# Performance work log

Hardware: AMD Instinct MI355X
Metric: run time of the kernel (lower is better)

Reference implementation:

```python
import jax, jax.numpy as jnp
import numpy as np

B, T, DIM = 2, 2048, 1024
H, DH, E, K = 16, 64, 8, 2


def setup_inputs() -> dict:
    key = jax.random.key(0)
    ks = jax.random.split(key, 7)
    s = 0.02
    return {
        "x":  jax.random.normal(ks[0], (B, T, DIM), jnp.float32),
        "Wq": jax.random.normal(ks[1], (H, DH, DIM), jnp.float32) * s,  # Linear(dim -> h*dh), reshaped
        "Wk": jax.random.normal(ks[2], (H, DH, DIM), jnp.float32) * s,
        "Wv": jax.random.normal(ks[3], (E, DH, DIM), jnp.float32) * s,  # per-expert Linear(dim -> dh)
        "Ws": jax.random.normal(ks[4], (H, E, DIM), jnp.float32) * s,   # V-gate Linear(dim -> h*e)
        "Wd": jax.random.normal(ks[5], (H, E, DIM), jnp.float32) * s,   # O-gate Linear(dim -> h*e)
        "Wo": jax.random.normal(ks[6], (E, DIM, DH), jnp.float32) * s,  # per-expert Linear(dh -> dim)
    }


def reference(x, Wq, Wk, Wv, Ws, Wd, Wo):
    scale = DH ** -0.5
    # projections: [b,h,t,dh]
    q = jnp.einsum('btc,hdc->bhtd', x, Wq)
    k = jnp.einsum('btc,hdc->bhtd', x, Wk)

    # ---- compute_moe (V experts): top-k gate, sigmoid weights ----
    gate_v = jnp.einsum('btc,hec->bthe', x, Ws)              # [b,t,h,e]
    w, sel = jax.lax.top_k(gate_v, K)                        # [b,t,h,K]
    wsig = jax.nn.sigmoid(w)
    oh = jax.nn.one_hot(sel, E, dtype=x.dtype)               # [b,t,h,K,e]
    mix_v = jnp.einsum('bthk,bthke->bthe', wsig, oh)         # weighted routing mask
    proj_v = jnp.einsum('btc,edc->bted', x, Wv)              # all-expert V projections (E small)
    v = jnp.einsum('bthe,bted->bhtd', mix_v, proj_v)         # [b,h,t,dh]

    # ---- standard attention core ----
    scores = jnp.einsum('bhid,bhjd->bhij', q * scale, k)     # [b,h,t,t]
    probs = jax.nn.softmax(scores, axis=-1)
    attn = jnp.einsum('bhij,bhjd->bihd', probs, v)           # [b,t,h,dh]

    # ---- compute_moe_o (O experts): top-k gate; NOTE original never uses its
    # softmax weights, so selected experts are summed UNWEIGHTED ----
    gate_o = jnp.einsum('btc,hec->bthe', x, Wd)
    _, sel_o = jax.lax.top_k(gate_o, K)
    mask_o = jax.nn.one_hot(sel_o, E, dtype=x.dtype).sum(axis=3)  # [b,t,h,e] in {0,1}
    res = jnp.einsum('bthe,bthd,efd->bthf', mask_o, attn, Wo)     # [b,t,h,dim]
    return res.sum(axis=2)                                        # [b,t,dim]
```

## Files before the change

kernel.cpp:

```cpp
#include <hip/hip_runtime.h>
#include <math.h>

#define TSEQ 2048
#define NB   2
#define NH   16
#define NE   8
#define DHD  64
#define MDIM 1024
#define MBT  4096
#define LDQKV 2560
#define GTAU 1e-3f
#define MAXFLAG 16384

typedef __attribute__((ext_vector_type(8))) short bf16x8;
typedef __attribute__((ext_vector_type(4))) float f32x4;
typedef __attribute__((ext_vector_type(16))) float f32x16;
typedef unsigned int u32;

__device__ inline unsigned short f2bf(float f) {
    union { float f; unsigned u; } v; v.f = f;
    unsigned r = v.u + 0x7fff + ((v.u >> 16) & 1);
    return (unsigned short)(r >> 16);
}
__device__ inline float bf2f(unsigned short h) {
    union { unsigned u; float f; } v; v.u = ((unsigned)h) << 16;
    return v.f;
}
__device__ inline u32 cvtpk(float a, float b) {
    u32 r;
    asm("v_cvt_pk_bf16_f32 %0, %1, %2" : "=v"(r) : "v"(a), "v"(b));
    return r;
}
__device__ inline float fexp2(float x) {
#if __has_builtin(__builtin_amdgcn_exp2f)
    return __builtin_amdgcn_exp2f(x);
#else
    float r; asm("v_exp_f32 %0, %1" : "=v"(r) : "v"(x)); return r;
#endif
}

__device__ inline void gload16(const void* g, void* l) {
    __builtin_amdgcn_global_load_lds((const __attribute__((address_space(1))) u32*)g,
                                     (__attribute__((address_space(3))) u32*)l, 16, 0, 0);
}

__device__ inline void cast8s(const float* __restrict__ in, unsigned short* __restrict__ out,
                              int i, float sc) {
    const float4* p = (const float4*)(in + (size_t)i * 8);
    float4 a = p[0], b = p[1];
    unsigned short o[8] = { f2bf(a.x*sc), f2bf(a.y*sc), f2bf(a.z*sc), f2bf(a.w*sc),
                            f2bf(b.x*sc), f2bf(b.y*sc), f2bf(b.z*sc), f2bf(b.w*sc) };
    *(uint4*)(out + (size_t)i * 8) = *(const uint4*)o;
}
__device__ inline void cast8hl(const float* __restrict__ in,
                               unsigned short* __restrict__ oh, unsigned short* __restrict__ ol,
                               int i) {
    const float4* p = (const float4*)(in + (size_t)i * 8);
    float4 a = p[0], b = p[1];
    float f[8] = { a.x, a.y, a.z, a.w, b.x, b.y, b.z, b.w };
    unsigned short h8[8], l8[8];
    #pragma unroll
    for (int j = 0; j < 8; ++j) {
        unsigned short hi = f2bf(f[j]);
        h8[j] = hi;
        l8[j] = f2bf(f[j] - bf2f(hi));
    }
    *(uint4*)(oh + (size_t)i * 8) = *(const uint4*)h8;
    *(uint4*)(ol + (size_t)i * 8) = *(const uint4*)l8;
}

__global__ __launch_bounds__(256)
void prep(const float* __restrict__ x,  const float* __restrict__ Wq,
          const float* __restrict__ Wk, const float* __restrict__ Wv,
          const float* __restrict__ Ws, const float* __restrict__ Wd,
          const float* __restrict__ Wo,
          unsigned short* __restrict__ xb, unsigned short* __restrict__ xbl,
          unsigned short* __restrict__ Wqkvb,
          unsigned short* __restrict__ Wsdh, unsigned short* __restrict__ Wsdl,
          unsigned short* __restrict__ WoTh, unsigned short* __restrict__ WoTl,
          u32* __restrict__ flags)
{
    const float qsc = 0.125f * 1.4426950408889634f;
    int b = blockIdx.x, tid = threadIdx.x;
    if (b == 0 && tid == 0) flags[0] = 0;
    if (b < 2048)      cast8hl(x, xb, xbl,          (b        ) * 256 + tid);
    else if (b < 2560) cast8s(Wq, Wqkvb,            (b - 2048) * 256 + tid, qsc);
    else if (b < 3072) cast8s(Wk, Wqkvb + 1048576,  (b - 2560) * 256 + tid, 1.f);
    else if (b < 3328) cast8s(Wv, Wqkvb + 2097152,  (b - 3072) * 256 + tid, 1.f);
    else if (b < 3456) {
        int i = (b - 3328) * 256 + tid;
        const float* src = (i < 16384) ? Ws + (size_t)i * 8 : Wd + (size_t)(i - 16384) * 8;
        const float4* p = (const float4*)src;
        float4 a = p[0], bq = p[1];
        float f8[8] = { a.x, a.y, a.z, a.w, bq.x, bq.y, bq.z, bq.w };
        unsigned short h8[8], l8[8];
        #pragma unroll
        for (int j = 0; j < 8; ++j) {
            unsigned short hi = f2bf(f8[j]);
            h8[j] = hi;
            l8[j] = f2bf(f8[j] - bf2f(hi));
        }
        *(uint4*)(Wsdh + (size_t)i * 8) = *(const uint4*)h8;
        *(uint4*)(Wsdl + (size_t)i * 8) = *(const uint4*)l8;
    } else {
        int idx = (b - 3456) * 256 + tid;
        int f = idx >> 9, ed = idx & 511, e = ed >> 6, d = ed & 63;
        float v = Wo[(size_t)e * (MDIM * DHD) + (size_t)f * DHD + d];
        unsigned short hi = f2bf(v);
        WoTh[idx] = hi;
        WoTl[idx] = f2bf(v - bf2f(hi));
    }
}

__global__ __launch_bounds__(256)
void mfma_gemm(const unsigned short* __restrict__ A,
               const unsigned short* __restrict__ B,
               unsigned short* __restrict__ C, int N, int K, int nbx)
{
    __shared__ __align__(16) unsigned short As[128 * 32];
    __shared__ __align__(16) unsigned short Bs[128 * 32];
    const int o = blockIdx.x;
    const int q8 = (int)gridDim.x >> 3;
    const int virt = (o & 7) * q8 + (o >> 3);
    const int bx = virt % nbx, by = virt / nbx;
    const int tid = threadIdx.x;
    const int lane = tid & 63, wave = tid >> 6;
    const int m0 = by * 128, n0 = bx * 128;
    const int wm = (wave >> 1) * 64, wn = (wave & 1) * 64;
    const int fr = lane & 15, fg = lane >> 4;
    const int grow = lane >> 2, gcol = (lane & 3) * 8;

    f32x4 acc[4][4];
    #pragma unroll
    for (int i = 0; i < 4; ++i)
        #pragma unroll
        for (int j = 0; j < 4; ++j) acc[i][j] = (f32x4)0.f;

    for (int k0 = 0; k0 < K; k0 += 32) {
        __syncthreads();
        const unsigned short* gA = A + (size_t)(m0 + wave * 32 + grow) * K + k0 + gcol;
        gload16(gA,                 As + wave * 1024);
        gload16(gA + (size_t)16 * K, As + wave * 1024 + 512);
        const unsigned short* gB = B + (size_t)(n0 + wave * 32 + grow) * K + k0 + gcol;
        gload16(gB,                 Bs + wave * 1024);
        gload16(gB + (size_t)16 * K, Bs + wave * 1024 + 512);
        __syncthreads();
        bf16x8 af[4], bfr[4];
        #pragma unroll
        for (int t = 0; t < 4; ++t) {
            af[t]  = *(const bf16x8*)(As + (wm + t * 16 + fr) * 32 + fg * 8);
            bfr[t] = *(const bf16x8*)(Bs + (wn + t * 16 + fr) * 32 + fg * 8);
        }
        #pragma unroll
        for (int i = 0; i < 4; ++i)
            #pragma unroll
            for (int j = 0; j < 4; ++j)
                acc[i][j] = __builtin_amdgcn_mfma_f32_16x16x32_bf16(af[i], bfr[j], acc[i][j], 0, 0, 0);
    }
    #pragma unroll
    for (int i = 0; i < 4; ++i)
        #pragma unroll
        for (int j = 0; j < 4; ++j)
            #pragma unroll
            for (int rr = 0; rr < 4; ++rr) {
                int row = m0 + wm + i * 16 + fg * 4 + rr;
                int col = n0 + wn + j * 16 + fr;
                C[(size_t)row * N + col] = f2bf(acc[i][j][rr]);
            }
}

__global__ __launch_bounds__(256)
void mfma_gemm3(const unsigned short* __restrict__ Ah, const unsigned short* __restrict__ Al,
                const unsigned short* __restrict__ Bh, const unsigned short* __restrict__ Bl,
                float* __restrict__ C)
{
    const int Kc = 512, N = 1024;
    __shared__ __align__(16) unsigned short Ash[128 * 32];
    __shared__ __align__(16) unsigned short Asl[128 * 32];
    __shared__ __align__(16) unsigned short Bsh[128 * 32];
    __shared__ __align__(16) unsigned short Bsl[128 * 32];
    const int o = blockIdx.x;
    const int virt = (o & 7) * 32 + (o >> 3);
    const int bx = virt & 7, by = virt >> 3;
    const int tid = threadIdx.x;
    const int lane = tid & 63, wave = tid >> 6;
    const int m0 = by * 128, n0 = bx * 128;
    const int wm = (wave >> 1) * 64, wn = (wave & 1) * 64;
    const int fr = lane & 15, fg = lane >> 4;
    const int grow = lane >> 2, gcol = (lane & 3) * 8;

    f32x4 acc[4][4];
    #pragma unroll
    for (int i = 0; i < 4; ++i)
        #pragma unroll
        for (int j = 0; j < 4; ++j) acc[i][j] = (f32x4)0.f;

    for (int k0 = 0; k0 < Kc; k0 += 32) {
        __syncthreads();
        const size_t roff  = (size_t)(m0 + wave * 32 + grow) * Kc + k0 + gcol;
        const size_t roffB = (size_t)(n0 + wave * 32 + grow) * Kc + k0 + gcol;
        gload16(Ah + roff,             Ash + wave * 1024);
        gload16(Ah + roff + 16 * Kc,   Ash + wave * 1024 + 512);
        gload16(Al + roff,             Asl + wave * 1024);
        gload16(Al + roff + 16 * Kc,   Asl + wave * 1024 + 512);
        gload16(Bh + roffB,            Bsh + wave * 1024);
        gload16(Bh + roffB + 16 * Kc,  Bsh + wave * 1024 + 512);
        gload16(Bl + roffB,            Bsl + wave * 1024);
        gload16(Bl + roffB + 16 * Kc,  Bsl + wave * 1024 + 512);
        __syncthreads();
        bf16x8 ah[4], al[4], bh[4], bl[4];
        #pragma unroll
        for (int t = 0; t < 4; ++t) {
            ah[t] = *(const bf16x8*)(Ash + (wm + t * 16 + fr) * 32 + fg * 8);
            al[t] = *(const bf16x8*)(Asl + (wm + t * 16 + fr) * 32 + fg * 8);
            bh[t] = *(const bf16x8*)(Bsh + (wn + t * 16 + fr) * 32 + fg * 8);
            bl[t] = *(const bf16x8*)(Bsl + (wn + t * 16 + fr) * 32 + fg * 8);
        }
        #pragma unroll
        for (int i = 0; i < 4; ++i)
            #pragma unroll
            for (int j = 0; j < 4; ++j) {
                acc[i][j] = __builtin_amdgcn_mfma_f32_16x16x32_bf16(ah[i], bh[j], acc[i][j], 0, 0, 0);
                acc[i][j] = __builtin_amdgcn_mfma_f32_16x16x32_bf16(ah[i], bl[j], acc[i][j], 0, 0, 0);
                acc[i][j] = __builtin_amdgcn_mfma_f32_16x16x32_bf16(al[i], bh[j], acc[i][j], 0, 0, 0);
            }
    }
    #pragma unroll
    for (int i = 0; i < 4; ++i)
        #pragma unroll
        for (int j = 0; j < 4; ++j)
            #pragma unroll
            for (int rr = 0; rr < 4; ++rr) {
                int row = m0 + wm + i * 16 + fg * 4 + rr;
                int col = n0 + wn + j * 16 + fr;
                C[(size_t)row * N + col] = acc[i][j][rr];
            }
}

__global__ __launch_bounds__(256)
void gate_gemm(const unsigned short* __restrict__ Ah, const unsigned short* __restrict__ Al,
               const unsigned short* __restrict__ Bh, const unsigned short* __restrict__ Bl,
               float* __restrict__ C)
{
    const int K = 1024, N = 256;
    __shared__ __align__(16) unsigned short S[4][64 * 32];
    const int tid = threadIdx.x;
    const int lane = tid & 63, wave = tid >> 6;
    const int m0 = blockIdx.y * 64, n0 = blockIdx.x * 64;
    const int wm = (wave >> 1) * 32, wn = (wave & 1) * 32;
    const int fr = lane & 15, fg = lane >> 4;
    const int grow = lane >> 2, gcol = (lane & 3) * 8;

    const unsigned short* src = (wave == 0) ? Ah : (wave == 1) ? Al : (wave == 2) ? Bh : Bl;
    const int brow = (wave >= 2) ? n0 : m0;

    f32x4 acc[2][2];
    #pragma unroll
    for (int i = 0; i < 2; ++i)
        #pragma unroll
        for (int j = 0; j < 2; ++j) acc[i][j] = (f32x4)0.f;

    for (int k0 = 0; k0 < K; k0 += 32) {
        __syncthreads();
        #pragma unroll
        for (int i = 0; i < 4; ++i)
            gload16(src + (size_t)(brow + i * 16 + grow) * K + k0 + gcol, &S[wave][i * 512]);
        __syncthreads();
        bf16x8 ah[2], al[2], bh[2], bl[2];
        #pragma unroll
        for (int t = 0; t < 2; ++t) {
            ah[t] = *(const bf16x8*)(&S[0][(wm + t * 16 + fr) * 32 + fg * 8]);
            al[t] = *(const bf16x8*)(&S[1][(wm + t * 16 + fr) * 32 + fg * 8]);
            bh[t] = *(const bf16x8*)(&S[2][(wn + t * 16 + fr) * 32 + fg * 8]);
            bl[t] = *(const bf16x8*)(&S[3][(wn + t * 16 + fr) * 32 + fg * 8]);
        }
        #pragma unroll
        for (int i = 0; i < 2; ++i)
            #pragma unroll
            for (int j = 0; j < 2; ++j) {
                acc[i][j] = __builtin_amdgcn_mfma_f32_16x16x32_bf16(ah[i], bh[j], acc[i][j], 0, 0, 0);
                acc[i][j] = __builtin_amdgcn_mfma_f32_16x16x32_bf16(ah[i], bl[j], acc[i][j], 0, 0, 0);
                acc[i][j] = __builtin_amdgcn_mfma_f32_16x16x32_bf16(al[i], bh[j], acc[i][j], 0, 0, 0);
            }
    }
    #pragma unroll
    for (int i = 0; i < 2; ++i)
        #pragma unroll
        for (int j = 0; j < 2; ++j)
            #pragma unroll
            for (int rr = 0; rr < 4; ++rr) {
                int row = m0 + wm + i * 16 + fg * 4 + rr;
                int col = n0 + wn + j * 16 + fr;
                C[(size_t)row * N + col] = acc[i][j][rr];
            }
}

__global__ __launch_bounds__(256)
void gate_topk2(const float* __restrict__ Gf,
                float2* __restrict__ wv, u32* __restrict__ selv, u32* __restrict__ selo,
                u32* __restrict__ flags)
{
    int item = blockIdx.x * 256 + threadIdx.x;
    int bt = item >> 4, h = item & 15;
    const float* g = Gf + (size_t)bt * 256 + h * NE;
    float b1 = -1e30f, b2 = -1e30f, b3 = -1e30f; int e1 = 0, e2 = 0;
    #pragma unroll
    for (int e = 0; e < NE; ++e) {
        float v = g[e];
        if (v > b1)      { b3 = b2; b2 = b1; e2 = e1; b1 = v; e1 = e; }
        else if (v > b2) { b3 = b2; b2 = v;  e2 = e; }
        else if (v > b3) { b3 = v; }
    }
    wv[item] = make_float2(1.f / (1.f + __expf(-b1)), 1.f / (1.f + __expf(-b2)));
    selv[item] = (u32)e1 | ((u32)e2 << 4);
    if (b2 - b3 < GTAU) {
        u32 p = atomicAdd(flags, 1u);
        if (p < MAXFLAG) flags[1 + p] = (u32)item;
    }
    const float* go = g + 128;
    float o1 = -1e30f, o2 = -1e30f, o3 = -1e30f; int f1 = 0, f2 = 0;
    #pragma unroll
    for (int e = 0; e < NE; ++e) {
        float v = go[e];
        if (v > o1)      { o3 = o2; o2 = o1; f2 = f1; o1 = v; f1 = e; }
        else if (v > o2) { o3 = o2; o2 = v;  f2 = e; }
        else if (v > o3) { o3 = v; }
    }
    selo[item] = (1u << f1) | (1u << f2);
    if (o2 - o3 < GTAU) {
        u32 p = atomicAdd(flags, 1u);
        if (p < MAXFLAG) flags[1 + p] = (u32)item | 0x10000u;
    }
}

__global__ __launch_bounds__(256)
void gate_fix(const float* __restrict__ x, const float* __restrict__ Ws,
              const float* __restrict__ Wd, const u32* __restrict__ flags,
              float2* __restrict__ wv, u32* __restrict__ selv, u32* __restrict__ selo)
{
    u32 nf = flags[0]; if (nf > MAXFLAG) nf = MAXFLAG;
    int gw = (blockIdx.x * 256 + threadIdx.x) >> 6;
    int lane = threadIdx.x & 63;
    int nwaves = gridDim.x * 4;
    for (u32 w = gw; w < nf; w += nwaves) {
        u32 rec = flags[1 + w];
        int item = rec & 0xffff, which = rec >> 16;
        int bt = item >> 4, h = item & 15;
        const float* W = (which ? Wd : Ws) + (size_t)h * NE * MDIM + lane * 16;
        const float* xr = x + (size_t)bt * MDIM + lane * 16;
        double g[8];
        #pragma unroll
        for (int e = 0; e < 8; ++e) {
            double s = 0.0;
            #pragma unroll
            for (int c = 0; c < 16; ++c)
                s += (double)xr[c] * (double)W[(size_t)e * MDIM + c];
            g[e] = s;
        }
        #pragma unroll
        for (int off = 32; off; off >>= 1)
            #pragma unroll
            for (int e = 0; e < 8; ++e)
                g[e] += __shfl_xor(g[e], off, 64);
        if (lane == 0) {
            double b1 = -1e300, b2 = -1e300; int i1 = 0, i2 = 0;
            #pragma unroll
            for (int e = 0; e < 8; ++e) {
                double v = g[e];
                if (v > b1)      { b2 = b1; i2 = i1; b1 = v; i1 = e; }
                else if (v > b2) { b2 = v;  i2 = e; }
            }
            if (which == 0) {
                wv[item] = make_float2(1.f / (1.f + __expf(-(float)b1)),
                                       1.f / (1.f + __expf(-(float)b2)));
                selv[item] = (u32)i1 | ((u32)i2 << 4);
            } else {
                selo[item] = (1u << i1) | (1u << i2);
            }
        }
    }
}

#define VTP 72
__global__ __launch_bounds__(256)
void vtrans(const unsigned short* __restrict__ QKVb, const float2* __restrict__ wv,
            const u32* __restrict__ selv, unsigned short* __restrict__ Vtg)
{
    __shared__ __align__(16) unsigned short Ls[256 * VTP];
    const int vid = blockIdx.x;
    const int xcd = vid & 7, local = vid >> 3;
    const int virt = xcd * 32 + local;
    const int b = virt >> 7, rem = virt & 127;
    const int tblk = rem >> 4, h = rem & 15;
    const int tid = threadIdx.x;

    {
        const int bt = b * TSEQ + tblk * 256 + tid;
        u32 s = selv[bt * 16 + h];
        float2 w = wv[bt * 16 + h];
        int e1 = s & 15, e2 = (s >> 4) & 15;
        const unsigned short* pv = QKVb + (size_t)bt * LDQKV + 2048;
        #pragma unroll
        for (int c = 0; c < 8; ++c) {
            uint4 a  = *(const uint4*)(pv + e1 * 64 + c * 8);
            uint4 bb = *(const uint4*)(pv + e2 * 64 + c * 8);
            unsigned short ea[8], eb[8], eo[8];
            *(uint4*)ea = a; *(uint4*)eb = bb;
            #pragma unroll
            for (int j = 0; j < 8; ++j)
                eo[j] = f2bf(w.x * bf2f(ea[j]) + w.y * bf2f(eb[j]));
            *(uint4*)(Ls + tid * VTP + c * 8) = *(const uint4*)eo;
        }
    }
    __syncthreads();
    {
        const int d = tid & 63, outer = tid >> 6;
        const size_t vrow = ((size_t)((b * NH + h) * DHD + d)) * TSEQ + tblk * 256;
        #pragma unroll
        for (int c8 = 0; c8 < 8; ++c8) {
            int t0 = (outer * 8 + c8) * 8;
            unsigned short o[8];
            #pragma unroll
            for (int j = 0; j < 8; ++j)
                o[j] = Ls[(t0 + j) * VTP + d];
            *(uint4*)(Vtg + vrow + t0) = *(const uint4*)o;
        }
    }
}

#define SPA 72
#define MFMA32(A,B,C) __builtin_amdgcn_mfma_f32_32x32x16_bf16(A, B, C, 0, 0, 0)
__global__ __launch_bounds__(256)
void attn_mfma(const unsigned short* __restrict__ QKVb,
               const unsigned short* __restrict__ Vtg,
               float* __restrict__ Op0, float* __restrict__ Op1,
               float* __restrict__ lp)
{
    __shared__ __align__(16) unsigned short Ks[64 * SPA];
    __shared__ __align__(16) unsigned short Vt[64 * SPA];
    const int vid = blockIdx.x;
    const int xcd = vid & 7, sl = vid >> 3;
    const int grp = xcd * 8 + (sl >> 4);
    const int q0  = (sl & 15) * 128;
    const int h   = grp & 15;
    const int z   = grp >> 4;
    const int b = z >> 1, split = z & 1;
    const int tid = threadIdx.x;
    const int lane = tid & 63, wq = tid >> 6;
    const int ql = lane & 31;
    const int hi = lane >> 5;
    const size_t base_q = ((size_t)b * TSEQ) * LDQKV + h * DHD;
    const size_t base_k = base_q + 1024;
    const size_t base_v = ((size_t)(b * NH + h) * DHD) * TSEQ;
    const int k00 = split * 1024;

    const int qrow = q0 + wq * 32 + ql;
    bf16x8 qa[4];
    #pragma unroll
    for (int t = 0; t < 4; ++t)
        qa[t] = *(const bf16x8*)(QKVb + base_q + (size_t)qrow * LDQKV + t * 16 + hi * 8);

    f32x16 o0 = (f32x16)0.f, o1 = (f32x16)0.f;
    float l_lane = 0.f;

    const int srow = tid >> 2, scol = (tid & 3) * 8;
    uint4 kr0 = *(const uint4*)(QKVb + base_k + (size_t)(k00 + srow) * LDQKV + scol);
    uint4 kr1 = *(const uint4*)(QKVb + base_k + (size_t)(k00 + srow) * LDQKV + scol + 32);
    uint4 vr0 = *(const uint4*)(Vtg + base_v + (size_t)srow * TSEQ + k00 + scol);
    uint4 vr1 = *(const uint4*)(Vtg + base_v + (size_t)srow * TSEQ + k00 + scol + 32);

    const int NT = 1024 / 64;
    for (int kb = 0; kb < NT; ++kb) {
        __syncthreads();
        *(uint4*)(Ks + srow * SPA + scol)      = kr0;
        *(uint4*)(Ks + srow * SPA + scol + 32) = kr1;
        *(uint4*)(Vt + srow * SPA + scol)      = vr0;
        *(uint4*)(Vt + srow * SPA + scol + 32) = vr1;
        __syncthreads();
        if (kb + 1 < NT) {
            const size_t gk = base_k + (size_t)(k00 + (kb + 1) * 64 + srow) * LDQKV + scol;
            const size_t gv = base_v + (size_t)srow * TSEQ + k00 + (kb + 1) * 64 + scol;
            kr0 = *(const uint4*)(QKVb + gk);
            kr1 = *(const uint4*)(QKVb + gk + 32);
            vr0 = *(const uint4*)(Vtg + gv);
            vr1 = *(const uint4*)(Vtg + gv + 32);
        }
        f32x16 s0 = (f32x16)0.f, s1 = (f32x16)0.f;
        #pragma unroll
        for (int t = 0; t < 4; ++t) {
            bf16x8 k0 = *(const bf16x8*)(Ks + ql * SPA + t * 16 + hi * 8);
            bf16x8 k1 = *(const bf16x8*)(Ks + (32 + ql) * SPA + t * 16 + hi * 8);
            s0 = MFMA32(k0, qa[t], s0);
            s1 = MFMA32(k1, qa[t], s1);
        }
        float ls0 = 0.f, ls1 = 0.f;
        u32 w[8];
        #pragma unroll
        for (int r = 0; r < 16; r += 2) {
            float pa = fexp2(s0[r]), pb = fexp2(s0[r + 1]);
            s0[r] = pa; s0[r + 1] = pb;
            ls0 += pa; ls1 += pb;
        }
        #pragma unroll
        for (int m = 0; m < 8; ++m) w[m] = cvtpk(s0[2*m], s0[2*m+1]);
        #pragma unroll
        for (int tl = 0; tl < 2; ++tl) {
            const int mb = 4 * tl, tk = tl;
            u32 send0 = hi ? w[mb]   : w[mb+2];
            u32 send1 = hi ? w[mb+1] : w[mb+3];
            u32 r0 = (u32)__shfl_xor((int)send0, 32, 64);
            u32 r1 = (u32)__shfl_xor((int)send1, 32, 64);
            union { u32 uw[4]; bf16x8 v; } pu;
            pu.uw[0] = hi ? r0 : w[mb];
            pu.uw[1] = hi ? r1 : w[mb+1];
            pu.uw[2] = hi ? w[mb+2] : r0;
            pu.uw[3] = hi ? w[mb+3] : r1;
            bf16x8 v0 = *(const bf16x8*)(Vt + ql * SPA + tk * 16 + hi * 8);
            bf16x8 v1 = *(const bf16x8*)(Vt + (32 + ql) * SPA + tk * 16 + hi * 8);
            o0 = MFMA32(pu.v, v0, o0);
            o1 = MFMA32(pu.v, v1, o1);
        }
        #pragma unroll
        for (int r = 0; r < 16; r += 2) {
            float pa = fexp2(s1[r]), pb = fexp2(s1[r + 1]);
            s1[r] = pa; s1[r + 1] = pb;
            ls0 += pa; ls1 += pb;
        }
        #pragma unroll
        for (int m = 0; m < 8; ++m) w[m] = cvtpk(s1[2*m], s1[2*m+1]);
        #pragma unroll
        for (int tl = 0; tl < 2; ++tl) {
            const int mb = 4 * tl, tk = 2 + tl;
            u32 send0 = hi ? w[mb]   : w[mb+2];
            u32 send1 = hi ? w[mb+1] : w[mb+3];
            u32 r0 = (u32)__shfl_xor((int)send0, 32, 64);
            u32 r1 = (u32)__shfl_xor((int)send1, 32, 64);
            union { u32 uw[4]; bf16x8 v; } pu;
            pu.uw[0] = hi ? r0 : w[mb];
            pu.uw[1] = hi ? r1 : w[mb+1];
            pu.uw[2] = hi ? w[mb+2] : r0;
            pu.uw[3] = hi ? w[mb+3] : r1;
            bf16x8 v0 = *(const bf16x8*)(Vt + ql * SPA + tk * 16 + hi * 8);
            bf16x8 v1 = *(const bf16x8*)(Vt + (32 + ql) * SPA + tk * 16 + hi * 8);
            o0 = MFMA32(pu.v, v0, o0);
            o1 = MFMA32(pu.v, v1, o1);
        }
        l_lane += ls0 + ls1;
    }
    float l_tot = l_lane + __shfl_xor(l_lane, 32, 64);
    float* Op = split ? Op1 : Op0;
    const size_t ob = ((size_t)b * TSEQ) * MDIM + h * DHD;
    #pragma unroll
    for (int r = 0; r < 16; ++r) {
        int qr = q0 + wq * 32 + (r & 3) + 8 * (r >> 2) + 4 * hi;
        Op[ob + (size_t)qr * MDIM + ql]      = o0[r];
        Op[ob + (size_t)qr * MDIM + 32 + ql] = o1[r];
    }
    if (hi == 0)
        lp[(((size_t)split * NB + b) * NH + h) * TSEQ + q0 + wq * 32 + ql] = l_tot;
}

__global__ __launch_bounds__(256)
void compute_U2(const float* __restrict__ Op0, const float* __restrict__ Op1,
                const float* __restrict__ lp, const u32* __restrict__ selo,
                unsigned short* __restrict__ Uh, unsigned short* __restrict__ Ul)
{
    int t = blockIdx.x * 256 + threadIdx.x;
    int bt = t >> 6, d = t & 63;
    int b = bt >> 11, ts = bt & 2047;
    float att[16];
    #pragma unroll
    for (int h = 0; h < NH; ++h) {
        size_t li = ((size_t)b * NH + h) * TSEQ + ts;
        float l = lp[li] + lp[li + (size_t)NB * NH * TSEQ];
        size_t oi = (size_t)bt * MDIM + h * DHD + d;
        att[h] = (Op0[oi] + Op1[oi]) / l;
    }
    const u32* sp = selo + bt * 16;
    u32 m[16];
    #pragma unroll
    for (int h = 0; h < NH; ++h) m[h] = sp[h];
    #pragma unroll
    for (int e = 0; e < NE; ++e) {
        float sum = 0.f;
        #pragma unroll
        for (int h = 0; h < NH; ++h)
            if (m[h] & (1u << e)) sum += att[h];
        int idx = bt * 512 + e * 64 + d;
        unsigned short hi16 = f2bf(sum);
        Uh[idx] = hi16;
        Ul[idx] = f2bf(sum - bf2f(hi16));
    }
}

extern "C" void kernel_launch(void* const* d_in, const int* in_sizes, int n_in,
                              void* d_out, int out_size, void* d_ws, size_t ws_size,
                              hipStream_t stream)
{
    const float* x  = (const float*)d_in[0];
    const float* Wq = (const float*)d_in[1];
    const float* Wk = (const float*)d_in[2];
    const float* Wv = (const float*)d_in[3];
    const float* Ws = (const float*)d_in[4];
    const float* Wd = (const float*)d_in[5];
    const float* Wo = (const float*)d_in[6];
    float* out = (float*)d_out;
    char* ws = (char*)d_ws;

    unsigned short* xb    = (unsigned short*)(ws);
    unsigned short* Wqkvb = (unsigned short*)(ws + 8388608);
    float*          Op0   = (float*)(ws);
    unsigned short* QKVb  = (unsigned short*)(ws + 16777216);
    unsigned short* Vtg   = (unsigned short*)(ws + 37748736);
    unsigned short* xbl   = (unsigned short*)(ws + 46137344);
    float*          Op1   = (float*)(ws + 46137344);
    float*          lp    = (float*)(ws + 62914560);
    unsigned short* WoTh  = (unsigned short*)(ws + 63438848);
    unsigned short* WoTl  = (unsigned short*)(ws + 64487424);
    float*          Gf    = (float*)(ws + 65536000);
    unsigned short* Uh    = (unsigned short*)(ws + 65536000);
    u32*            flags = (u32*)(ws + 69730304);
    unsigned short* Ul    = (unsigned short*)(ws + 69730304);
    float2*         wvp   = (float2*)(ws + 73924608);
    u32*            selv  = (u32*)(ws + 74448896);
    u32*            selo  = (u32*)(ws + 74711040);
    unsigned short* Wsdh  = (unsigned short*)(ws + 74973184);
    unsigned short* Wsdl  = (unsigned short*)(ws + 75497472);

    dim3 blk(256);
    prep<<<5504, blk, 0, stream>>>(x, Wq, Wk, Wv, Ws, Wd, Wo,
                                   xb, xbl, Wqkvb, Wsdh, Wsdl, WoTh, WoTl, flags);

    mfma_gemm<<<640, blk, 0, stream>>>(xb, Wqkvb, QKVb, LDQKV, 1024, 20);

    gate_gemm<<<dim3(4, 64), blk, 0, stream>>>(xb, xbl, Wsdh, Wsdl, Gf);
    gate_topk2<<<256, blk, 0, stream>>>(Gf, wvp, selv, selo, flags);
    gate_fix<<<64, blk, 0, stream>>>(x, Ws, Wd, flags, wvp, selv, selo);

    vtrans<<<256, blk, 0, stream>>>(QKVb, wvp, selv, Vtg);

    attn_mfma<<<1024, blk, 0, stream>>>(QKVb, Vtg, Op0, Op1, lp);

    compute_U2<<<1024, blk, 0, stream>>>(Op0, Op1, lp, selo, Uh, Ul);
    mfma_gemm3<<<256, blk, 0, stream>>>(Uh, Ul, WoTh, WoTl, out);
}
```

Baseline: 178.6 us.

## Fold gate projection into QKV GEMM with single-bf16 and wider fp32 fixup

The separate three-pass split-bf16 gate GEMM is removed. The Ws/Wd gate weights are appended as extra columns of the QKV weight matrix, so one GEMM launch produces Q, K, V and the gate logits, with the gate columns stored as fp32. Because gate logits are now computed in plain bf16, the top-k tie tolerance is widened and the fp32 fixup kernel gets more blocks and a larger flag capacity to recheck ambiguous routings. This saves a launch and the hi/lo conversions of x, but more tokens may need the exact fp32 recompute.

```diff
diff --git a/kernel.cpp b/kernel.cpp
--- a/kernel.cpp
+++ b/kernel.cpp
@@ -9,8 +9,9 @@
 #define MDIM 1024
 #define MBT  4096
 #define LDQKV 2560
-#define GTAU 1e-3f
-#define MAXFLAG 16384
+#define NFULL 2816
+#define GTAU 1.2e-2f
+#define MAXFLAG 32768
 
 typedef __attribute__((ext_vector_type(8))) short bf16x8;
 typedef __attribute__((ext_vector_type(4))) float f32x4;
@@ -52,38 +53,20 @@
                             f2bf(b.x*sc), f2bf(b.y*sc), f2bf(b.z*sc), f2bf(b.w*sc) };
     *(uint4*)(out + (size_t)i * 8) = *(const uint4*)o;
 }
-__device__ inline void cast8hl(const float* __restrict__ in,
-                               unsigned short* __restrict__ oh, unsigned short* __restrict__ ol,
-                               int i) {
-    const float4* p = (const float4*)(in + (size_t)i * 8);
-    float4 a = p[0], b = p[1];
-    float f[8] = { a.x, a.y, a.z, a.w, b.x, b.y, b.z, b.w };
-    unsigned short h8[8], l8[8];
-    #pragma unroll
-    for (int j = 0; j < 8; ++j) {
-        unsigned short hi = f2bf(f[j]);
-        h8[j] = hi;
-        l8[j] = f2bf(f[j] - bf2f(hi));
-    }
-    *(uint4*)(oh + (size_t)i * 8) = *(const uint4*)h8;
-    *(uint4*)(ol + (size_t)i * 8) = *(const uint4*)l8;
-}
 
 __global__ __launch_bounds__(256)
 void prep(const float* __restrict__ x,  const float* __restrict__ Wq,
           const float* __restrict__ Wk, const float* __restrict__ Wv,
           const float* __restrict__ Ws, const float* __restrict__ Wd,
           const float* __restrict__ Wo,
-          unsigned short* __restrict__ xb, unsigned short* __restrict__ xbl,
-          unsigned short* __restrict__ Wqkvb,
-          unsigned short* __restrict__ Wsdh, unsigned short* __restrict__ Wsdl,
+          unsigned short* __restrict__ xb, unsigned short* __restrict__ Wqkvb,
           unsigned short* __restrict__ WoTh, unsigned short* __restrict__ WoTl,
           u32* __restrict__ flags)
 {
     const float qsc = 0.125f * 1.4426950408889634f;
     int b = blockIdx.x, tid = threadIdx.x;
     if (b == 0 && tid == 0) flags[0] = 0;
-    if (b < 2048)      cast8hl(x, xb, xbl,          (b        ) * 256 + tid);
+    if (b < 2048)      cast8s(x,  xb,               (b        ) * 256 + tid, 1.f);
     else if (b < 2560) cast8s(Wq, Wqkvb,            (b - 2048) * 256 + tid, qsc);
     else if (b < 3072) cast8s(Wk, Wqkvb + 1048576,  (b - 2560) * 256 + tid, 1.f);
     else if (b < 3328) cast8s(Wv, Wqkvb + 2097152,  (b - 3072) * 256 + tid, 1.f);
@@ -92,16 +75,9 @@
         const float* src = (i < 16384) ? Ws + (size_t)i * 8 : Wd + (size_t)(i - 16384) * 8;
         const float4* p = (const float4*)src;
         float4 a = p[0], bq = p[1];
-        float f8[8] = { a.x, a.y, a.z, a.w, bq.x, bq.y, bq.z, bq.w };
-        unsigned short h8[8], l8[8];
-        #pragma unroll
-        for (int j = 0; j < 8; ++j) {
-            unsigned short hi = f2bf(f8[j]);
-            h8[j] = hi;
-            l8[j] = f2bf(f8[j] - bf2f(hi));
-        }
-        *(uint4*)(Wsdh + (size_t)i * 8) = *(const uint4*)h8;
-        *(uint4*)(Wsdl + (size_t)i * 8) = *(const uint4*)l8;
+        unsigned short o[8] = { f2bf(a.x), f2bf(a.y), f2bf(a.z), f2bf(a.w),
+                                f2bf(bq.x), f2bf(bq.y), f2bf(bq.z), f2bf(bq.w) };
+        *(uint4*)(Wqkvb + 2621440 + (size_t)i * 8) = *(const uint4*)o;
     } else {
         int idx = (b - 3456) * 256 + tid;
         int f = idx >> 9, ed = idx & 511, e = ed >> 6, d = ed & 63;
@@ -113,10 +89,11 @@
 }
 
 __global__ __launch_bounds__(256)
-void mfma_gemm(const unsigned short* __restrict__ A,
-               const unsigned short* __restrict__ B,
-               unsigned short* __restrict__ C, int N, int K, int nbx)
-{
+void qkv_gemm(const unsigned short* __restrict__ A,
+              const unsigned short* __restrict__ B,
+              unsigned short* __restrict__ Cb, float* __restrict__ Gf)
+{
+    const int K = 1024, nbx = 22;
     __shared__ __align__(16) unsigned short As[128 * 32];
     __shared__ __align__(16) unsigned short Bs[128 * 32];
     const int o = blockIdx.x;
@@ -157,16 +134,29 @@
             for (int j = 0; j < 4; ++j)
                 acc[i][j] = __builtin_amdgcn_mfma_f32_16x16x32_bf16(af[i], bfr[j], acc[i][j], 0, 0, 0);
     }
-    #pragma unroll
-    for (int i = 0; i < 4; ++i)
-        #pragma unroll
-        for (int j = 0; j < 4; ++j)
-            #pragma unroll
-            for (int rr = 0; rr < 4; ++rr) {
-                int row = m0 + wm + i * 16 + fg * 4 + rr;
-                int col = n0 + wn + j * 16 + fr;
-                C[(size_t)row * N + col] = f2bf(acc[i][j][rr]);
-            }
+    if (n0 < LDQKV) {
+        #pragma unroll
+        for (int i = 0; i < 4; ++i)
+            #pragma unroll
+            for (int j = 0; j < 4; ++j)
+                #pragma unroll
+                for (int rr = 0; rr < 4; ++rr) {
+                    int row = m0 + wm + i * 16 + fg * 4 + rr;
+                    int col = n0 + wn + j * 16 + fr;
+                    Cb[(size_t)row * LDQKV + col] = f2bf(acc[i][j][rr]);
+                }
+    } else {
+        #pragma unroll
+        for (int i = 0; i < 4; ++i)
+            #pragma unroll
+            for (int j = 0; j < 4; ++j)
+                #pragma unroll
+                for (int rr = 0; rr < 4; ++rr) {
+                    int row = m0 + wm + i * 16 + fg * 4 + rr;
+                    int col = n0 - LDQKV + wn + j * 16 + fr;
+                    Gf[(size_t)row * 256 + col] = acc[i][j][rr];
+                }
+    }
 }
 
 __global__ __launch_bounds__(256)
@@ -229,64 +219,6 @@
     for (int i = 0; i < 4; ++i)
         #pragma unroll
         for (int j = 0; j < 4; ++j)
-            #pragma unroll
-            for (int rr = 0; rr < 4; ++rr) {
-                int row = m0 + wm + i * 16 + fg * 4 + rr;
-                int col = n0 + wn + j * 16 + fr;
-                C[(size_t)row * N + col] = acc[i][j][rr];
-            }
-}
-
-__global__ __launch_bounds__(256)
-void gate_gemm(const unsigned short* __restrict__ Ah, const unsigned short* __restrict__ Al,
-               const unsigned short* __restrict__ Bh, const unsigned short* __restrict__ Bl,
-               float* __restrict__ C)
-{
-    const int K = 1024, N = 256;
-    __shared__ __align__(16) unsigned short S[4][64 * 32];
-    const int tid = threadIdx.x;
-    const int lane = tid & 63, wave = tid >> 6;
-    const int m0 = blockIdx.y * 64, n0 = blockIdx.x * 64;
-    const int wm = (wave >> 1) * 32, wn = (wave & 1) * 32;
-    const int fr = lane & 15, fg = lane >> 4;
-    const int grow = lane >> 2, gcol = (lane & 3) * 8;
-
-    const unsigned short* src = (wave == 0) ? Ah : (wave == 1) ? Al : (wave == 2) ? Bh : Bl;
-    const int brow = (wave >= 2) ? n0 : m0;
-
-    f32x4 acc[2][2];
-    #pragma unroll
-    for (int i = 0; i < 2; ++i)
-        #pragma unroll
-        for (int j = 0; j < 2; ++j) acc[i][j] = (f32x4)0.f;
-
-    for (int k0 = 0; k0 < K; k0 += 32) {
-        __syncthreads();
-        #pragma unroll
-        for (int i = 0; i < 4; ++i)
-            gload16(src + (size_t)(brow + i * 16 + grow) * K + k0 + gcol, &S[wave][i * 512]);
-        __syncthreads();
-        bf16x8 ah[2], al[2], bh[2], bl[2];
-        #pragma unroll
-        for (int t = 0; t < 2; ++t) {
-            ah[t] = *(const bf16x8*)(&S[0][(wm + t * 16 + fr) * 32 + fg * 8]);
-            al[t] = *(const bf16x8*)(&S[1][(wm + t * 16 + fr) * 32 + fg * 8]);
-            bh[t] = *(const bf16x8*)(&S[2][(wn + t * 16 + fr) * 32 + fg * 8]);
-            bl[t] = *(const bf16x8*)(&S[3][(wn + t * 16 + fr) * 32 + fg * 8]);
-        }
-        #pragma unroll
-        for (int i = 0; i < 2; ++i)
-            #pragma unroll
-            for (int j = 0; j < 2; ++j) {
-                acc[i][j] = __builtin_amdgcn_mfma_f32_16x16x32_bf16(ah[i], bh[j], acc[i][j], 0, 0, 0);
-                acc[i][j] = __builtin_amdgcn_mfma_f32_16x16x32_bf16(ah[i], bl[j], acc[i][j], 0, 0, 0);
-                acc[i][j] = __builtin_amdgcn_mfma_f32_16x16x32_bf16(al[i], bh[j], acc[i][j], 0, 0, 0);
-            }
-    }
-    #pragma unroll
-    for (int i = 0; i < 2; ++i)
-        #pragma unroll
-        for (int j = 0; j < 2; ++j)
             #pragma unroll
             for (int rr = 0; rr < 4; ++rr) {
                 int row = m0 + wm + i * 16 + fg * 4 + rr;
@@ -612,7 +544,6 @@
     float*          Op0   = (float*)(ws);
     unsigned short* QKVb  = (unsigned short*)(ws + 16777216);
     unsigned short* Vtg   = (unsigned short*)(ws + 37748736);
-    unsigned short* xbl   = (unsigned short*)(ws + 46137344);
     float*          Op1   = (float*)(ws + 46137344);
     float*          lp    = (float*)(ws + 62914560);
     unsigned short* WoTh  = (unsigned short*)(ws + 63438848);
@@ -624,18 +555,15 @@
     float2*         wvp   = (float2*)(ws + 73924608);
     u32*            selv  = (u32*)(ws + 74448896);
     u32*            selo  = (u32*)(ws + 74711040);
-    unsigned short* Wsdh  = (unsigned short*)(ws + 74973184);
-    unsigned short* Wsdl  = (unsigned short*)(ws + 75497472);
 
     dim3 blk(256);
     prep<<<5504, blk, 0, stream>>>(x, Wq, Wk, Wv, Ws, Wd, Wo,
-                                   xb, xbl, Wqkvb, Wsdh, Wsdl, WoTh, WoTl, flags);
-
-    mfma_gemm<<<640, blk, 0, stream>>>(xb, Wqkvb, QKVb, LDQKV, 1024, 20);
-
-    gate_gemm<<<dim3(4, 64), blk, 0, stream>>>(xb, xbl, Wsdh, Wsdl, Gf);
+                                   xb, Wqkvb, WoTh, WoTl, flags);
+
+    qkv_gemm<<<704, blk, 0, stream>>>(xb, Wqkvb, QKVb, Gf);
+
     gate_topk2<<<256, blk, 0, stream>>>(Gf, wvp, selv, selo, flags);
-    gate_fix<<<64, blk, 0, stream>>>(x, Ws, Wd, flags, wvp, selv, selo);
+    gate_fix<<<512, blk, 0, stream>>>(x, Ws, Wd, flags, wvp, selv, selo);
 
     vtrans<<<256, blk, 0, stream>>>(QKVb, wvp, selv, Vtg);
 
```

Result: slower. 201.4 us (+12.8%).
